# Optimization experiments

Hardware: AMD Instinct MI355X
Metric: run time of the kernel (lower is better)

The kernel has to match this reference:

```python
import jax, jax.numpy as jnp
import numpy as np

MASK_VALUE = -1000000.0


def setup_inputs() -> dict:
    key = jax.random.key(0)
    k1, k2, k3, k4 = jax.random.split(key, 4)
    B, Lq, Lk, d = 32, 1024, 1024, 128
    return {
        "query": jax.random.normal(k1, (B, Lq, d), dtype=jnp.float32),
        "key": jax.random.normal(k2, (B, Lk, d), dtype=jnp.float32),
        "value": jax.random.normal(k3, (B, Lk, d), dtype=jnp.float32),
        "valid_length": jax.random.randint(k4, (B,), 0, Lk, dtype=jnp.int64),
    }


def reference(query, key, value, valid_length):
    # query [B, Lq, d], key/value [B, Lk, d], valid_length [B]
    d = query.shape[-1]
    # scores [B, Lq, Lk]
    scores = jnp.einsum("bqd,bkd->bqk", query, key) / jnp.sqrt(jnp.float32(d))
    Lk = key.shape[1]
    # mask positions >= valid_length with -1e6 (per-batch, broadcast over Lq)
    pos = jnp.arange(Lk)  # [Lk]
    mask = pos[None, None, :] >= valid_length[:, None, None]  # [B, 1, Lk]
    scores = jnp.where(mask, MASK_VALUE, scores)
    attn = jax.nn.softmax(scores, axis=-1)
    # dropout p=0.0 in eval -> identity
    return jnp.einsum("bqk,bkd->bqd", attn, value)
```

## Files before the change

kernel.cpp:

```cpp
#include <hip/hip_runtime.h>

#define B_N 32
#define LQ  1024
#define LK  1024
#define DH  128

typedef __attribute__((ext_vector_type(4))) float f32x4;
typedef __attribute__((ext_vector_type(8))) short s16x8;

__device__ inline unsigned short f2bf(float f) {
    union { float f; unsigned u; } c; c.f = f;
    unsigned u = c.u;
    u += 0x7fffu + ((u >> 16) & 1u);
    return (unsigned short)(u >> 16);
}

#define ESCALE 0.12751743f

__global__ __launch_bounds__(256)
void prep_kv(const float* __restrict__ K, const float* __restrict__ V,
             unsigned short* __restrict__ Kb, unsigned short* __restrict__ Vt)
{
    __shared__ float tl[32 * 132];
    const int tid  = threadIdx.x;
    const int lane = tid & 63;
    const int wv   = tid >> 6;
    const int n    = lane & 15;
    const int quad = lane >> 4;

    const bool isK = blockIdx.x < 1024;
    const int  t   = isK ? blockIdx.x : (blockIdx.x - 1024);
    const int  b   = t >> 5, kt = t & 31;

    const float4* src = (const float4*)((isK ? K : V) + ((size_t)b * LK + kt * 32) * DH);
    #pragma unroll
    for (int h = 0; h < 4; ++h) {
        const int idx = h * 256 + tid;
        const int row = idx >> 5, c4 = idx & 31;
        *(float4*)&tl[row * 132 + c4 * 4] = src[idx];
    }
    __syncthreads();

    union { s16x8 v; unsigned short u[8]; } t8;
    if (isK) {
        #pragma unroll
        for (int h = 0; h < 2; ++h) {
            const int f = wv * 2 + h;
            const int tt2 = f >> 2, s = f & 3;
            const float* p = &tl[(tt2 * 16 + n) * 132 + s * 32 + quad * 8];
            const float4 a = *(const float4*)p;
            const float4 c = *(const float4*)(p + 4);
            t8.u[0] = f2bf(a.x); t8.u[1] = f2bf(a.y); t8.u[2] = f2bf(a.z); t8.u[3] = f2bf(a.w);
            t8.u[4] = f2bf(c.x); t8.u[5] = f2bf(c.y); t8.u[6] = f2bf(c.z); t8.u[7] = f2bf(c.w);
            const int w = b * 256 + (kt * 2 + tt2) * 4 + s;
            *(s16x8*)(Kb + (size_t)w * 512 + lane * 8) = t8.v;
        }
    } else {
        #pragma unroll
        for (int h = 0; h < 2; ++h) {
            const int c8 = wv * 2 + h;
            #pragma unroll
            for (int j = 0; j < 8; ++j)
                t8.u[j] = f2bf(tl[(quad * 8 + j) * 132 + c8 * 16 + n]);
            const int v = b * 256 + kt * 8 + c8;
            *(s16x8*)(Vt + (size_t)v * 512 + lane * 8) = t8.v;
        }
    }
}

#define PSTRIDE 72

__global__ __launch_bounds__(64)
void attn_fwd(const float* __restrict__ Q, const unsigned short* __restrict__ Kb,
              const unsigned short* __restrict__ Vt, const int* __restrict__ VL,
              float* __restrict__ O)
{
    __shared__ unsigned short Plds[16 * PSTRIDE];

    const int lane = threadIdx.x & 63;
    const int quad = lane >> 4;
    const int m16  = lane & 15;

    const int b  = blockIdx.x & 31;
    const int qt = blockIdx.x >> 5;
    const int q0 = qt * 16;

    const int vl = VL[b];
    const int nch = (vl > 0) ? ((vl + 63) >> 6) : 16;
    const float emaskval = (vl == 0) ? 1.0f : 0.0f;

    s16x8 qf[4];
    {
        const float* qrow = Q + ((size_t)b * LQ + q0 + m16) * DH + quad * 8;
        #pragma unroll
        for (int s = 0; s < 4; ++s) {
            const float4 a = *(const float4*)(qrow + s * 32);
            const float4 c = *(const float4*)(qrow + s * 32 + 4);
            union { s16x8 v; unsigned short u[8]; } t;
            t.u[0] = f2bf(a.x); t.u[1] = f2bf(a.y); t.u[2] = f2bf(a.z); t.u[3] = f2bf(a.w);
            t.u[4] = f2bf(c.x); t.u[5] = f2bf(c.y); t.u[6] = f2bf(c.z); t.u[7] = f2bf(c.w);
            qf[s] = t.v;
        }
    }

    f32x4 o[8];
    #pragma unroll
    for (int c8 = 0; c8 < 8; ++c8) o[c8] = (f32x4){0.f, 0.f, 0.f, 0.f};
    float lrun[4] = {0.f, 0.f, 0.f, 0.f};

    const unsigned short* kbase = Kb + (size_t)b * (256 * 512) + lane * 8;
    const unsigned short* vbase = Vt + (size_t)b * (256 * 512) + lane * 8;

    s16x8 kf[16], vfA[8], vfB[8];
    #pragma unroll
    for (int i = 0; i < 16; ++i) kf[i] = *(const s16x8*)(kbase + i * 512);
    #pragma unroll
    for (int i = 0; i < 8; ++i) vfA[i] = *(const s16x8*)(vbase + i * 512);
    #pragma unroll
    for (int i = 0; i < 8; ++i) vfB[i] = *(const s16x8*)(vbase + (8 + i) * 512);

    for (int kb = 0; kb < nch; ++kb) {
        f32x4 st[4];
        #pragma unroll
        for (int tn = 0; tn < 4; ++tn) st[tn] = (f32x4){0.f, 0.f, 0.f, 0.f};
        #pragma unroll
        for (int tn = 0; tn < 4; ++tn) {
            #pragma unroll
            for (int s = 0; s < 4; ++s)
                st[tn] = __builtin_amdgcn_mfma_f32_16x16x32_bf16(qf[s], kf[tn * 4 + s], st[tn], 0, 0, 0);
        }

        const int knx = (kb + 1 < nch) ? (kb + 1) : kb;
        const unsigned short* kcn = kbase + (size_t)knx * (16 * 512);
        #pragma unroll
        for (int i = 0; i < 16; ++i) kf[i] = *(const s16x8*)(kcn + i * 512);

        const bool maskc = (kb * 64 + 64 > vl);
        #pragma unroll
        for (int r = 0; r < 4; ++r) {
            float e[4];
            #pragma unroll
            for (int tn = 0; tn < 4; ++tn) {
                e[tn] = __builtin_amdgcn_exp2f(st[tn][r] * ESCALE);
                if (maskc && (kb * 64 + tn * 16 + m16 >= vl)) e[tn] = emaskval;
            }
            lrun[r] += (e[0] + e[1]) + (e[2] + e[3]);
            const int prow = (quad * 4 + r) * PSTRIDE;
            #pragma unroll
            for (int tn = 0; tn < 4; ++tn) Plds[prow + tn * 16 + m16] = f2bf(e[tn]);
        }

        __asm__ volatile("s_waitcnt lgkmcnt(0)" ::: "memory");
        const s16x8 pf0 = *(const s16x8*)&Plds[m16 * PSTRIDE + quad * 8];
        const s16x8 pf1 = *(const s16x8*)&Plds[m16 * PSTRIDE + 32 + quad * 8];

        const unsigned short* vcn = vbase + (size_t)knx * (16 * 512);

        #pragma unroll
        for (int c8 = 0; c8 < 8; ++c8)
            o[c8] = __builtin_amdgcn_mfma_f32_16x16x32_bf16(pf0, vfA[c8], o[c8], 0, 0, 0);
        #pragma unroll
        for (int i = 0; i < 8; ++i) vfA[i] = *(const s16x8*)(vcn + i * 512);
        #pragma unroll
        for (int c8 = 0; c8 < 8; ++c8)
            o[c8] = __builtin_amdgcn_mfma_f32_16x16x32_bf16(pf1, vfB[c8], o[c8], 0, 0, 0);
        #pragma unroll
        for (int i = 0; i < 8; ++i) vfB[i] = *(const s16x8*)(vcn + (8 + i) * 512);
    }

    const size_t obase = ((size_t)b * LQ + q0 + quad * 4) * DH + m16;
    #pragma unroll
    for (int r = 0; r < 4; ++r) {
        float L = lrun[r];
        L += __shfl_xor(L, 1);
        L += __shfl_xor(L, 2);
        L += __shfl_xor(L, 4);
        L += __shfl_xor(L, 8);
        const float inv = 1.0f / L;
        #pragma unroll
        for (int c8 = 0; c8 < 8; ++c8)
            O[obase + (size_t)r * DH + c8 * 16] = o[c8][r] * inv;
    }
}

extern "C" void kernel_launch(void* const* d_in, const int* in_sizes, int n_in,
                              void* d_out, int out_size, void* d_ws, size_t ws_size,
                              hipStream_t stream) {
    const float* Q  = (const float*)d_in[0];
    const float* K  = (const float*)d_in[1];
    const float* V  = (const float*)d_in[2];
    const int*   VL = (const int*)d_in[3];
    float* O = (float*)d_out;
    (void)in_sizes; (void)n_in; (void)out_size; (void)ws_size;

    unsigned short* Kb = (unsigned short*)d_ws;
    unsigned short* Vt = Kb + (size_t)B_N * 256 * 512;

    prep_kv<<<dim3(2048), dim3(256), 0, stream>>>(K, V, Kb, Vt);
    attn_fwd<<<dim3(B_N * (LQ / 16)), dim3(64), 0, stream>>>(Q, Kb, Vt, VL, O);
}
```

Measured before the change: 129.0 us.

## Compute transposed scores so P feeds PV MFMA from registers, skipping LDS

The QK^T MFMA now has its operands swapped, so the score tile comes out transposed and each lane already holds the P fragment in the layout the PV multiply needs. This removes the LDS round-trip for P, including the shared-memory store, the wait and the reloads. V is repacked in the prep kernel as fp16 in a matching layout, and the PV product uses 16x16x16 f16 MFMAs in place of 16x16x32 bf16. The row-sum reduction changes from per-row shuffles to a cross-quad reduce followed by a broadcast; the cost is twice as many, smaller MFMA instructions for PV.

```diff
diff --git a/kernel.cpp b/kernel.cpp
--- a/kernel.cpp
+++ b/kernel.cpp
@@ -5,8 +5,10 @@
 #define LK  1024
 #define DH  128
 
-typedef __attribute__((ext_vector_type(4))) float f32x4;
-typedef __attribute__((ext_vector_type(8))) short s16x8;
+typedef __attribute__((ext_vector_type(4))) float    f32x4;
+typedef __attribute__((ext_vector_type(8))) short    s16x8;
+typedef __attribute__((ext_vector_type(4))) _Float16 f16x4;
+typedef __attribute__((ext_vector_type(8))) _Float16 f16x8;
 
 __device__ inline unsigned short f2bf(float f) {
     union { float f; unsigned u; } c; c.f = f;
@@ -19,7 +21,7 @@
 
 __global__ __launch_bounds__(256)
 void prep_kv(const float* __restrict__ K, const float* __restrict__ V,
-             unsigned short* __restrict__ Kb, unsigned short* __restrict__ Vt)
+             unsigned short* __restrict__ Kb, _Float16* __restrict__ Vt)
 {
     __shared__ float tl[32 * 132];
     const int tid  = threadIdx.x;
@@ -41,8 +43,8 @@
     }
     __syncthreads();
 
-    union { s16x8 v; unsigned short u[8]; } t8;
     if (isK) {
+        union { s16x8 v; unsigned short u[8]; } t8;
         #pragma unroll
         for (int h = 0; h < 2; ++h) {
             const int f = wv * 2 + h;
@@ -58,25 +60,26 @@
     } else {
         #pragma unroll
         for (int h = 0; h < 2; ++h) {
-            const int c8 = wv * 2 + h;
+            const int f  = wv * 2 + h;
+            const int kg = f >> 2, dp = f & 3;
+            f16x8 t8;
             #pragma unroll
-            for (int j = 0; j < 8; ++j)
-                t8.u[j] = f2bf(tl[(quad * 8 + j) * 132 + c8 * 16 + n]);
-            const int v = b * 256 + kt * 8 + c8;
-            *(s16x8*)(Vt + (size_t)v * 512 + lane * 8) = t8.v;
+            for (int i = 0; i < 4; ++i) {
+                const float* row = &tl[(kg * 16 + quad * 4 + i) * 132 + dp * 32 + n];
+                t8[i]     = (_Float16)row[0];
+                t8[4 + i] = (_Float16)row[16];
+            }
+            const int v = (b * 64 + kt * 2 + kg) * 4 + dp;
+            *(f16x8*)(Vt + (size_t)v * 512 + lane * 8) = t8;
         }
     }
 }
 
-#define PSTRIDE 72
-
 __global__ __launch_bounds__(64)
 void attn_fwd(const float* __restrict__ Q, const unsigned short* __restrict__ Kb,
-              const unsigned short* __restrict__ Vt, const int* __restrict__ VL,
+              const _Float16* __restrict__ Vt, const int* __restrict__ VL,
               float* __restrict__ O)
 {
-    __shared__ unsigned short Plds[16 * PSTRIDE];
-
     const int lane = threadIdx.x & 63;
     const int quad = lane >> 4;
     const int m16  = lane & 15;
@@ -105,29 +108,28 @@
 
     f32x4 o[8];
     #pragma unroll
-    for (int c8 = 0; c8 < 8; ++c8) o[c8] = (f32x4){0.f, 0.f, 0.f, 0.f};
-    float lrun[4] = {0.f, 0.f, 0.f, 0.f};
+    for (int dt = 0; dt < 8; ++dt) o[dt] = (f32x4){0.f, 0.f, 0.f, 0.f};
+    float lrun = 0.f;
 
     const unsigned short* kbase = Kb + (size_t)b * (256 * 512) + lane * 8;
-    const unsigned short* vbase = Vt + (size_t)b * (256 * 512) + lane * 8;
+    const _Float16*       vbase = Vt + (size_t)b * (256 * 512) + lane * 8;
 
-    s16x8 kf[16], vfA[8], vfB[8];
+    s16x8 kf[16];
+    f16x8 vp[16];
     #pragma unroll
     for (int i = 0; i < 16; ++i) kf[i] = *(const s16x8*)(kbase + i * 512);
     #pragma unroll
-    for (int i = 0; i < 8; ++i) vfA[i] = *(const s16x8*)(vbase + i * 512);
-    #pragma unroll
-    for (int i = 0; i < 8; ++i) vfB[i] = *(const s16x8*)(vbase + (8 + i) * 512);
+    for (int i = 0; i < 16; ++i) vp[i] = *(const f16x8*)(vbase + i * 512);
 
     for (int kb = 0; kb < nch; ++kb) {
         f32x4 st[4];
         #pragma unroll
-        for (int tn = 0; tn < 4; ++tn) st[tn] = (f32x4){0.f, 0.f, 0.f, 0.f};
+        for (int g = 0; g < 4; ++g) st[g] = (f32x4){0.f, 0.f, 0.f, 0.f};
         #pragma unroll
-        for (int tn = 0; tn < 4; ++tn) {
+        for (int g = 0; g < 4; ++g) {
             #pragma unroll
             for (int s = 0; s < 4; ++s)
-                st[tn] = __builtin_amdgcn_mfma_f32_16x16x32_bf16(qf[s], kf[tn * 4 + s], st[tn], 0, 0, 0);
+                st[g] = __builtin_amdgcn_mfma_f32_16x16x32_bf16(kf[g * 4 + s], qf[s], st[g], 0, 0, 0);
         }
 
         const int knx = (kb + 1 < nch) ? (kb + 1) : kb;
@@ -136,50 +138,46 @@
         for (int i = 0; i < 16; ++i) kf[i] = *(const s16x8*)(kcn + i * 512);
 
         const bool maskc = (kb * 64 + 64 > vl);
+        f16x4 pA[4];
         #pragma unroll
-        for (int r = 0; r < 4; ++r) {
+        for (int g = 0; g < 4; ++g) {
             float e[4];
             #pragma unroll
-            for (int tn = 0; tn < 4; ++tn) {
-                e[tn] = __builtin_amdgcn_exp2f(st[tn][r] * ESCALE);
-                if (maskc && (kb * 64 + tn * 16 + m16 >= vl)) e[tn] = emaskval;
+            for (int i = 0; i < 4; ++i) {
+                e[i] = __builtin_amdgcn_exp2f(st[g][i] * ESCALE);
+                if (maskc && (kb * 64 + g * 16 + quad * 4 + i >= vl)) e[i] = emaskval;
             }
-            lrun[r] += (e[0] + e[1]) + (e[2] + e[3]);
-            const int prow = (quad * 4 + r) * PSTRIDE;
-            #pragma unroll
-            for (int tn = 0; tn < 4; ++tn) Plds[prow + tn * 16 + m16] = f2bf(e[tn]);
+            lrun += (e[0] + e[1]) + (e[2] + e[3]);
+            pA[g] = (f16x4){(_Float16)e[0], (_Float16)e[1], (_Float16)e[2], (_Float16)e[3]};
         }
 
-        __asm__ volatile("s_waitcnt lgkmcnt(0)" ::: "memory");
-        const s16x8 pf0 = *(const s16x8*)&Plds[m16 * PSTRIDE + quad * 8];
-        const s16x8 pf1 = *(const s16x8*)&Plds[m16 * PSTRIDE + 32 + quad * 8];
+        #pragma unroll
+        for (int g = 0; g < 4; ++g) {
+            #pragma unroll
+            for (int dp = 0; dp < 4; ++dp) {
+                const f16x8 w  = vp[g * 4 + dp];
+                const f16x4 lo = __builtin_shufflevector(w, w, 0, 1, 2, 3);
+                const f16x4 hi = __builtin_shufflevector(w, w, 4, 5, 6, 7);
+                o[dp * 2]     = __builtin_amdgcn_mfma_f32_16x16x16f16(pA[g], lo, o[dp * 2],     0, 0, 0);
+                o[dp * 2 + 1] = __builtin_amdgcn_mfma_f32_16x16x16f16(pA[g], hi, o[dp * 2 + 1], 0, 0, 0);
+            }
+        }
 
-        const unsigned short* vcn = vbase + (size_t)knx * (16 * 512);
-
+        const _Float16* vcn = vbase + (size_t)knx * (16 * 512);
         #pragma unroll
-        for (int c8 = 0; c8 < 8; ++c8)
-            o[c8] = __builtin_amdgcn_mfma_f32_16x16x32_bf16(pf0, vfA[c8], o[c8], 0, 0, 0);
-        #pragma unroll
-        for (int i = 0; i < 8; ++i) vfA[i] = *(const s16x8*)(vcn + i * 512);
-        #pragma unroll
-        for (int c8 = 0; c8 < 8; ++c8)
-            o[c8] = __builtin_amdgcn_mfma_f32_16x16x32_bf16(pf1, vfB[c8], o[c8], 0, 0, 0);
-        #pragma unroll
-        for (int i = 0; i < 8; ++i) vfB[i] = *(const s16x8*)(vcn + (8 + i) * 512);
+        for (int i = 0; i < 16; ++i) vp[i] = *(const f16x8*)(vcn + i * 512);
     }
 
+    float L = lrun;
+    L += __shfl_xor(L, 16);
+    L += __shfl_xor(L, 32);
     const size_t obase = ((size_t)b * LQ + q0 + quad * 4) * DH + m16;
     #pragma unroll
     for (int r = 0; r < 4; ++r) {
-        float L = lrun[r];
-        L += __shfl_xor(L, 1);
-        L += __shfl_xor(L, 2);
-        L += __shfl_xor(L, 4);
-        L += __shfl_xor(L, 8);
-        const float inv = 1.0f / L;
+        const float inv = 1.0f / __shfl(L, quad * 4 + r);
         #pragma unroll
-        for (int c8 = 0; c8 < 8; ++c8)
-            O[obase + (size_t)r * DH + c8 * 16] = o[c8][r] * inv;
+        for (int dt = 0; dt < 8; ++dt)
+            O[obase + (size_t)r * DH + dt * 16] = o[dt][r] * inv;
     }
 }
 
@@ -194,7 +192,7 @@
     (void)in_sizes; (void)n_in; (void)out_size; (void)ws_size;
 
     unsigned short* Kb = (unsigned short*)d_ws;
-    unsigned short* Vt = Kb + (size_t)B_N * 256 * 512;
+    _Float16*       Vt = (_Float16*)(Kb + (size_t)B_N * 256 * 512);
 
     prep_kv<<<dim3(2048), dim3(256), 0, stream>>>(K, V, Kb, Vt);
     attn_fwd<<<dim3(B_N * (LQ / 16)), dim3(64), 0, stream>>>(Q, Kb, Vt, VL, O);
```

After: 131.2 us. Within noise of the previous version (+1.7%).
